# Kernel optimization log

Hardware: AMD Instinct MI355X
Metric: run time of the kernel (lower is better)

The kernel has to match this reference:

```python
import jax, jax.numpy as jnp
import numpy as np

D_MODEL = 1024
H = 16
D_K = D_MODEL // H  # 64


def setup_inputs() -> dict:
    key = jax.random.key(0)
    ks = jax.random.split(key, 10)
    s = 1.0 / np.sqrt(D_MODEL)
    x = jax.random.normal(ks[0], (4, 2048, D_MODEL), dtype=jnp.float32)
    # Per-head linear weights stacked: [H, d_model, d_k]
    Wq = jax.random.uniform(ks[1], (H, D_MODEL, D_K), jnp.float32, -s, s)
    bq = jax.random.uniform(ks[2], (H, D_K), jnp.float32, -s, s)
    Wk = jax.random.uniform(ks[3], (H, D_MODEL, D_K), jnp.float32, -s, s)
    bk = jax.random.uniform(ks[4], (H, D_K), jnp.float32, -s, s)
    Wv = jax.random.uniform(ks[5], (H, D_MODEL, D_K), jnp.float32, -s, s)
    bv = jax.random.uniform(ks[6], (H, D_K), jnp.float32, -s, s)
    so = 1.0 / np.sqrt(H * D_K)
    Wo = jax.random.uniform(ks[7], (H * D_K, D_MODEL), jnp.float32, -so, so)
    bo = jax.random.uniform(ks[8], (D_MODEL,), jnp.float32, -so, so)
    return {"x": x, "Wq": Wq, "bq": bq, "Wk": Wk, "bk": bk, "Wv": Wv, "bv": bv, "Wo": Wo, "bo": bo}


def reference(x, Wq, bq, Wk, bk, Wv, bv, Wo, bo):
    # x: [B, S, D]; Wq/Wk/Wv: [H, D, d_k]; b*: [H, d_k]
    q = jnp.einsum('bsd,hdk->bhsk', x, Wq) + bq[None, :, None, :]
    k = jnp.einsum('bsd,hdk->bhsk', x, Wk) + bk[None, :, None, :]
    v = jnp.einsum('bsd,hdk->bhsk', x, Wv) + bv[None, :, None, :]
    scores = jnp.einsum('bhqk,bhsk->bhqs', q, k) / np.sqrt(D_K)
    S = x.shape[1]
    causal = jnp.triu(jnp.ones((S, S), dtype=bool), k=1)  # True above diagonal
    scores = jnp.where(causal, -jnp.inf, scores)
    attn = jax.nn.softmax(scores, axis=-1)
    ctx = jnp.einsum('bhqs,bhsk->bhqk', attn, v)  # [B, H, S, d_k]
    B = x.shape[0]
    # concat heads: torch cats head outputs along last dim -> [B, S, H*d_k]
    ctx = jnp.transpose(ctx, (0, 2, 1, 3)).reshape(B, S, H * D_K)
    return ctx @ Wo + bo
```

## Files before the change

kernel.cpp:

```cpp
#include <hip/hip_runtime.h>
#include <hip/hip_bf16.h>

typedef unsigned short u16;
typedef __attribute__((ext_vector_type(8))) short short8;
typedef __attribute__((ext_vector_type(4))) short short4v;
typedef __attribute__((ext_vector_type(4))) float floatx4;

#define D_MODEL 1024
#define NH 16
#define SEQ 2048
#define BATCH 4
#define M_ROWS 8192
#define N_QKV 3072

#define QSCALE 0.18033688011112042f
#define EXP2_OFF 11.541560327111707f

__device__ __forceinline__ u16 f2u(float f) {
    __hip_bfloat16 h = __float2bfloat16(f);
    u16 u; __builtin_memcpy(&u, &h, 2); return u;
}

__device__ __forceinline__ void async_copy16(const u16* g, u16* l) {
    __builtin_amdgcn_global_load_lds(
        (const __attribute__((address_space(1))) unsigned int*)(g),
        (__attribute__((address_space(3))) unsigned int*)(l),
        16, 0, 0);
}

__global__ __launch_bounds__(256) void prep(
    const float* __restrict__ x,
    const float* __restrict__ Wq, const float* __restrict__ Wk,
    const float* __restrict__ Wv, const float* __restrict__ Wo,
    const float* __restrict__ bq, const float* __restrict__ bk,
    const float* __restrict__ bv, const float* __restrict__ bo,
    u16* __restrict__ xb, u16* __restrict__ Wpt, u16* __restrict__ Wot,
    float* __restrict__ biasp)
{
    __shared__ u16 T[64 * 72];
    const int tid = threadIdx.x;
    const int blk = blockIdx.x;

    if (blk < 4096) {
        size_t i = ((size_t)blk * 256 + tid) * 8;
        float4 f0 = *(const float4*)&x[i];
        float4 f1 = *(const float4*)&x[i + 4];
        u16 t[8] = {f2u(f0.x), f2u(f0.y), f2u(f0.z), f2u(f0.w),
                    f2u(f1.x), f2u(f1.y), f2u(f1.z), f2u(f1.w)};
        *(short8*)&xb[i] = *(short8*)t;
        return;
    }
    if (blk == 5120) {
        #pragma unroll
        for (int j = 0; j < 16; j++) {
            int idx = j * 256 + tid;
            float v;
            if (idx < 1024)      v = bq[idx] * QSCALE;
            else if (idx < 2048) v = bk[idx - 1024];
            else if (idx < 3072) v = bv[idx - 2048];
            else                 v = bo[idx - 3072];
            biasp[idx] = v;
        }
        return;
    }
    const int wb = blk - 4096;
    const int r = tid >> 2, s4 = (tid & 3) * 16;
    if (wb < 768) {
        int sel = wb / 256, rem = wb % 256;
        int h = rem >> 4, ktile = rem & 15;
        const float* W = (sel == 0) ? Wq : ((sel == 1) ? Wk : Wv);
        const float scale = (sel == 0) ? QSCALE : 1.0f;
        const float* src = W + ((size_t)h * 1024 + ktile * 64 + r) * 64 + s4;
        #pragma unroll
        for (int i = 0; i < 16; i++) T[(s4 + i) * 72 + r] = f2u(src[i] * scale);
        __syncthreads();
        u16 tmp[16];
        #pragma unroll
        for (int i = 0; i < 16; i++) tmp[i] = T[r * 72 + s4 + i];
        u16* dst = Wpt + ((size_t)sel * 1024 + h * 64 + r) * 1024 + ktile * 64 + s4;
        *(short8*)&dst[0] = *(short8*)&tmp[0];
        *(short8*)&dst[8] = *(short8*)&tmp[8];
    } else {
        int rem = wb - 768;
        int nt = rem >> 4, kt2 = rem & 15;
        const float* src = Wo + ((size_t)kt2 * 64 + r) * 1024 + nt * 64 + s4;
        #pragma unroll
        for (int i = 0; i < 16; i++) T[(s4 + i) * 72 + r] = f2u(src[i]);
        __syncthreads();
        u16 tmp[16];
        #pragma unroll
        for (int i = 0; i < 16; i++) tmp[i] = T[r * 72 + s4 + i];
        u16* dst = Wot + ((size_t)nt * 64 + r) * 1024 + kt2 * 64 + s4;
        *(short8*)&dst[0] = *(short8*)&tmp[0];
        *(short8*)&dst[8] = *(short8*)&tmp[8];
    }
}

__global__ __launch_bounds__(256) void vtrans(const u16* __restrict__ QKV,
                                              u16* __restrict__ Vtg) {
    __shared__ u16 T[64 * 72];
    const int bh = blockIdx.x, kt = blockIdx.y;
    const int b = bh >> 4, h = bh & 15;
    const int tid = threadIdx.x;
    const int r = tid >> 2, s4 = (tid & 3) * 16;
    const u16* vp = QKV + (size_t)(b * SEQ + kt * 64 + r) * N_QKV + 2 * D_MODEL + h * 64 + s4;
    *(short8*)&T[r * 72 + s4]     = *(const short8*)&vp[0];
    *(short8*)&T[r * 72 + s4 + 8] = *(const short8*)&vp[8];
    __syncthreads();
    u16 tmp[16];
    #pragma unroll
    for (int i = 0; i < 16; i++) tmp[i] = T[(s4 + i) * 72 + r];
    u16* op = Vtg + ((size_t)bh * 64 + r) * SEQ + kt * 64 + s4;
    *(short8*)&op[0] = *(short8*)&tmp[0];
    *(short8*)&op[8] = *(short8*)&tmp[8];
}

#define G256_BAR   __builtin_amdgcn_s_barrier()
#define G256_LGKM(n) { asm volatile("s_waitcnt lgkmcnt(" #n ")" ::: "memory"); \
                       __builtin_amdgcn_sched_barrier(0); }

#define GQ_STAGE_A(bb, ca, kq) \
    async_copy16(pAc + (size_t)(ca) * 64 * K + (kq), \
                 &lds[(bb) * 28672 + (ca) * 4096 + stw]);

#define GQ_STAGE_B(bb, cb, kq) \
    async_copy16(pBc + (size_t)(cb) * 64 * K + (kq), \
                 &lds[(bb) * 28672 + 16384 + (cb) * 4096 + stw]);

#define GQ_LDA4(dst, bb, mi0) { \
    const int _b = (bb) * 28672 + wm * 8192; \
    _Pragma("unroll") \
    for (int mi = 0; mi < 4; mi++) { \
        const int _r = _b + (((mi0) + mi) * 16 + l16) * 64; \
        dst[mi * 2]     = *(const short8*)&lds[_r + col0]; \
        dst[mi * 2 + 1] = *(const short8*)&lds[_r + col1]; \
    } }

#define GQ_LDB2(dst, bb, ni0) { \
    const int _b = (bb) * 28672 + 16384 + wn * 3072; \
    _Pragma("unroll") \
    for (int ni = 0; ni < 2; ni++) { \
        const int _r = _b + (((ni0) + ni) * 16 + l16) * 64; \
        dst[ni * 2]     = *(const short8*)&lds[_r + col0]; \
        dst[ni * 2 + 1] = *(const short8*)&lds[_r + col1]; \
    } }

#define GQ_LDB1(dst, bb, ni0) { \
    const int _b = (bb) * 28672 + 16384 + wn * 3072; \
    const int _r = _b + ((ni0) * 16 + l16) * 64; \
    dst[0] = *(const short8*)&lds[_r + col0]; \
    dst[1] = *(const short8*)&lds[_r + col1]; }

#define GQ_MMA8(av, bv, MI0, NI0) { \
    _Pragma("unroll") \
    for (int mi = 0; mi < 4; mi++) \
    _Pragma("unroll") \
    for (int ni = 0; ni < 2; ni++) { \
        acc[(MI0) + mi][(NI0) + ni] = __builtin_amdgcn_mfma_f32_16x16x32_bf16( \
            bv[ni * 2],     av[mi * 2],     acc[(MI0) + mi][(NI0) + ni], 0, 0, 0); \
        acc[(MI0) + mi][(NI0) + ni] = __builtin_amdgcn_mfma_f32_16x16x32_bf16( \
            bv[ni * 2 + 1], av[mi * 2 + 1], acc[(MI0) + mi][(NI0) + ni], 0, 0, 0); \
    } }

#define GQ_MMA4(av, bv, MI0) { \
    _Pragma("unroll") \
    for (int mi = 0; mi < 4; mi++) { \
        acc[(MI0) + mi][2] = __builtin_amdgcn_mfma_f32_16x16x32_bf16( \
            bv[0], av[mi * 2],     acc[(MI0) + mi][2], 0, 0, 0); \
        acc[(MI0) + mi][2] = __builtin_amdgcn_mfma_f32_16x16x32_bf16( \
            bv[1], av[mi * 2 + 1], acc[(MI0) + mi][2], 0, 0, 0); \
    } }

template <typename OT>
__global__ __launch_bounds__(512, 2) void gemm_qkv(
    const u16* __restrict__ A, const u16* __restrict__ Bt,
    const float* __restrict__ bias, OT* __restrict__ C,
    int M, int N, int K)
{
    __shared__ u16 lds[57344];
    const int tid = threadIdx.x;
    const int w = tid >> 6, lane = tid & 63;
    const int l16 = lane & 15, quad = lane >> 4;
    const int wm = w >> 2, wn = w & 3;

    const int nwgx = gridDim.x;
    const int nwg = nwgx * gridDim.y;
    const int lin = blockIdx.y * nwgx + blockIdx.x;
    const int cpx = nwg >> 3;
    const int swz = (lin & 7) * cpx + (lin >> 3);
    const int bn = (swz % nwgx) * 192, bm = (swz / nwgx) * 256;

    const int d = tid * 16;
    const int s = d ^ (((d >> 7) & 7) << 4);
    const int r = s >> 7;
    const int c = (s & 127) >> 1;
    const u16* pAc = A  + (size_t)(bm + r) * K + c;
    const u16* pBc = Bt + (size_t)(bn + r) * K + c;
    const int stw = w * 512;

    const int xm = (l16 & 7) << 3;
    const int col0 = (quad * 8) ^ xm;
    const int col1 = (32 + quad * 8) ^ xm;

    floatx4 acc[8][3];
    #pragma unroll
    for (int i = 0; i < 8; i++)
        #pragma unroll
        for (int j = 0; j < 3; j++) acc[i][j] = (floatx4){0.f, 0.f, 0.f, 0.f};

    GQ_STAGE_A(0, 0, 0); GQ_STAGE_A(0, 1, 0); GQ_STAGE_A(0, 2, 0); GQ_STAGE_A(0, 3, 0);
    GQ_STAGE_B(0, 0, 0); GQ_STAGE_B(0, 1, 0); GQ_STAGE_B(0, 2, 0);
    GQ_STAGE_B(1, 0, 64); GQ_STAGE_B(1, 1, 64); GQ_STAGE_B(1, 2, 64);
    asm volatile("s_waitcnt vmcnt(3)" ::: "memory");
    __syncthreads();

    short8 a0[8], a1[8], b0[4], b1[2];
    GQ_LDA4(a0, 0, 0);
    GQ_LDB2(b0, 0, 0);

    const int NKT = K >> 6;
    for (int kt = 0; kt < NKT; ++kt) {
        const int buf = kt & 1, nb = buf ^ 1;
        const int kqA = (kt + 1) << 6, kqB = (kt + 2) << 6;
        const bool st1 = (kt + 1 < NKT), st2 = (kt + 2 < NKT);

        GQ_LDB1(b1, buf, 2);
        if (st1) { GQ_STAGE_A(nb, 0, kqA); GQ_STAGE_A(nb, 1, kqA); }
        G256_BAR; G256_LGKM(2);
        __builtin_amdgcn_s_setprio(1); GQ_MMA8(a0, b0, 0, 0);
        __builtin_amdgcn_s_setprio(0); G256_BAR;

        GQ_LDA4(a1, buf, 4);
        if (st1) { GQ_STAGE_A(nb, 2, kqA); GQ_STAGE_A(nb, 3, kqA); }
        G256_BAR; G256_LGKM(8);
        __builtin_amdgcn_s_setprio(1); GQ_MMA4(a0, b1, 0);
        __builtin_amdgcn_s_setprio(0); G256_BAR;

        if (st2) { GQ_STAGE_B(buf, 0, kqB); GQ_STAGE_B(buf, 1, kqB); }
        G256_BAR; G256_LGKM(0);
        __builtin_amdgcn_s_setprio(1); GQ_MMA8(a1, b0, 4, 0);
        __builtin_amdgcn_s_setprio(0); G256_BAR;

        if (st2) { GQ_STAGE_B(buf, 2, kqB); }
        if (st1) {
            if (st2) { asm volatile("s_waitcnt vmcnt(3)" ::: "memory"); }
            else     { asm volatile("s_waitcnt vmcnt(0)" ::: "memory"); }
            __builtin_amdgcn_sched_barrier(0);
            GQ_LDA4(a0, nb, 0);
            GQ_LDB2(b0, nb, 0);
        }
        G256_BAR;
        __builtin_amdgcn_s_setprio(1); GQ_MMA4(a1, b1, 4);
        __builtin_amdgcn_s_setprio(0); G256_BAR;
    }

    float4 bi[3];
    #pragma unroll
    for (int ni = 0; ni < 3; ni++)
        bi[ni] = *(const float4*)&bias[bn + wn * 48 + ni * 16 + quad * 4];
    #pragma unroll
    for (int mi = 0; mi < 8; mi++) {
        const int row = bm + wm * 128 + mi * 16 + l16;
        #pragma unroll
        for (int ni = 0; ni < 3; ni++) {
            const int col = bn + wn * 48 + ni * 16 + quad * 4;
            const float v0 = acc[mi][ni][0] + bi[ni].x;
            const float v1 = acc[mi][ni][1] + bi[ni].y;
            const float v2 = acc[mi][ni][2] + bi[ni].z;
            const float v3 = acc[mi][ni][3] + bi[ni].w;
            if constexpr (sizeof(OT) == 2) {
                u16 o[4] = {f2u(v0), f2u(v1), f2u(v2), f2u(v3)};
                *(short4v*)&((u16*)C)[(size_t)row * N + col] = *(short4v*)o;
            } else {
                float4 fv = {v0, v1, v2, v3};
                *(float4*)&C[(size_t)row * N + col] = fv;
            }
        }
    }
}

#define GO_STAGE_A(bb, ca, kq) \
    async_copy16(pAc + (size_t)(ca) * 64 * K + (kq), \
                 &lds[(bb) * 24576 + (ca) * 4096 + stw]);

#define GO_STAGE_B(bb, cb, kq) \
    async_copy16(pBc + (size_t)(cb) * 64 * K + (kq), \
                 &lds[(bb) * 24576 + 16384 + (cb) * 4096 + stw]);

#define GO_LDA4(dst, bb, mi0) { \
    const int _b = (bb) * 24576 + wm * 8192; \
    _Pragma("unroll") \
    for (int mi = 0; mi < 4; mi++) { \
        const int _r = _b + (((mi0) + mi) * 16 + l16) * 64; \
        dst[mi * 2]     = *(const short8*)&lds[_r + col0]; \
        dst[mi * 2 + 1] = *(const short8*)&lds[_r + col1]; \
    } }

#define GO_LDB1(dst, bb, ni) { \
    const int _b = (bb) * 24576 + 16384; \
    const int _r = _b + (wn * 32 + (ni) * 16 + l16) * 64; \
    dst[0] = *(const short8*)&lds[_r + col0]; \
    dst[1] = *(const short8*)&lds[_r + col1]; }

#define GO_MMA(av, bv, MI0, NI) { \
    _Pragma("unroll") \
    for (int mi = 0; mi < 4; mi++) { \
        acc[(MI0) + mi][NI] = __builtin_amdgcn_mfma_f32_16x16x32_bf16( \
            bv[0], av[mi * 2],     acc[(MI0) + mi][NI], 0, 0, 0); \
        acc[(MI0) + mi][NI] = __builtin_amdgcn_mfma_f32_16x16x32_bf16( \
            bv[1], av[mi * 2 + 1], acc[(MI0) + mi][NI], 0, 0, 0); \
    } }

__global__ __launch_bounds__(512, 2) void gemm_out(
    const u16* __restrict__ A, const u16* __restrict__ Bt,
    const float* __restrict__ bias, float* __restrict__ C,
    int M, int N, int K)
{
    __shared__ u16 lds[49152];
    const int tid = threadIdx.x;
    const int w = tid >> 6, lane = tid & 63;
    const int l16 = lane & 15, quad = lane >> 4;
    const int wm = w >> 2, wn = w & 3;

    const int nwgx = gridDim.x;
    const int nwg = nwgx * gridDim.y;
    const int lin = blockIdx.y * nwgx + blockIdx.x;
    const int cpx = nwg >> 3;
    const int swz = (lin & 7) * cpx + (lin >> 3);
    const int bn = (swz % nwgx) * 128, bm = (swz / nwgx) * 256;

    const int d = tid * 16;
    const int s = d ^ (((d >> 7) & 7) << 4);
    const int r = s >> 7;
    const int c = (s & 127) >> 1;
    const u16* pAc = A  + (size_t)(bm + r) * K + c;
    const u16* pBc = Bt + (size_t)(bn + r) * K + c;
    const int stw = w * 512;

    const int xm = (l16 & 7) << 3;
    const int col0 = (quad * 8) ^ xm;
    const int col1 = (32 + quad * 8) ^ xm;

    floatx4 acc[8][2];
    #pragma unroll
    for (int i = 0; i < 8; i++)
        #pragma unroll
        for (int j = 0; j < 2; j++) acc[i][j] = (floatx4){0.f, 0.f, 0.f, 0.f};

    GO_STAGE_A(0, 0, 0); GO_STAGE_A(0, 1, 0); GO_STAGE_A(0, 2, 0); GO_STAGE_A(0, 3, 0);
    GO_STAGE_B(0, 0, 0); GO_STAGE_B(0, 1, 0);
    GO_STAGE_B(1, 0, 64); GO_STAGE_B(1, 1, 64);
    asm volatile("s_waitcnt vmcnt(2)" ::: "memory");
    __syncthreads();

    short8 a0[8], a1[8], bb0[2], bb1[2];
    GO_LDA4(a0, 0, 0);
    GO_LDB1(bb0, 0, 0);

    const int NKT = K >> 6;
    for (int kt = 0; kt < NKT; ++kt) {
        const int buf = kt & 1, nb = buf ^ 1;
        const int kqA = (kt + 1) << 6, kqB = (kt + 2) << 6;
        const bool st1 = (kt + 1 < NKT), st2 = (kt + 2 < NKT);

        GO_LDB1(bb1, buf, 1);
        if (st1) { GO_STAGE_A(nb, 0, kqA); GO_STAGE_A(nb, 1, kqA); }
        G256_BAR; G256_LGKM(2);
        __builtin_amdgcn_s_setprio(1); GO_MMA(a0, bb0, 0, 0);
        __builtin_amdgcn_s_setprio(0); G256_BAR;

        GO_LDA4(a1, buf, 4);
        if (st1) { GO_STAGE_A(nb, 2, kqA); GO_STAGE_A(nb, 3, kqA); }
        G256_BAR; G256_LGKM(8);
        __builtin_amdgcn_s_setprio(1); GO_MMA(a0, bb1, 0, 1);
        __builtin_amdgcn_s_setprio(0); G256_BAR;

        if (st2) { GO_STAGE_B(buf, 0, kqB); GO_STAGE_B(buf, 1, kqB); }
        G256_BAR; G256_LGKM(0);
        __builtin_amdgcn_s_setprio(1); GO_MMA(a1, bb0, 4, 0);
        __builtin_amdgcn_s_setprio(0); G256_BAR;

        if (st1) {
            if (st2) { asm volatile("s_waitcnt vmcnt(2)" ::: "memory"); }
            else     { asm volatile("s_waitcnt vmcnt(0)" ::: "memory"); }
            __builtin_amdgcn_sched_barrier(0);
            GO_LDA4(a0, nb, 0);
            GO_LDB1(bb0, nb, 0);
        }
        G256_BAR;
        __builtin_amdgcn_s_setprio(1); GO_MMA(a1, bb1, 4, 1);
        __builtin_amdgcn_s_setprio(0); G256_BAR;
    }

    float4 bi[2];
    #pragma unroll
    for (int ni = 0; ni < 2; ni++)
        bi[ni] = *(const float4*)&bias[bn + wn * 32 + ni * 16 + quad * 4];
    #pragma unroll
    for (int mi = 0; mi < 8; mi++) {
        const int row = bm + wm * 128 + mi * 16 + l16;
        #pragma unroll
        for (int ni = 0; ni < 2; ni++) {
            const int col = bn + wn * 32 + ni * 16 + quad * 4;
            float4 fv = {acc[mi][ni][0] + bi[ni].x, acc[mi][ni][1] + bi[ni].y,
                         acc[mi][ni][2] + bi[ni].z, acc[mi][ni][3] + bi[ni].w};
            *(float4*)&C[(size_t)row * N + col] = fv;
        }
    }
}

__global__ __launch_bounds__(256) void attn_mfma(
    const u16* __restrict__ QKV, const u16* __restrict__ Vtg, u16* __restrict__ ctx)
{
    __shared__ u16 Ks[2][64 * 64];
    __shared__ u16 Vs[2][64 * 64];
    __shared__ u16 Ps[4 * 16 * 64];

    const int bh = blockIdx.x;
    const int qt = (int)(gridDim.y - 1) - (int)blockIdx.y;
    const int b = bh >> 4, h = bh & 15;
    const int tid = threadIdx.x;
    const int w = tid >> 6, lane = tid & 63;
    const int l16 = lane & 15, quad = lane >> 4;

    const int r0 = tid >> 3,        c0 = tid & 7;
    const int r1 = (256 + tid) >> 3, c1 = tid & 7;
    const int sw0 = c0 ^ (r0 & 7), sw1 = c1 ^ (r1 & 7);

    short8 q[2][2];
    #pragma unroll
    for (int m = 0; m < 2; m++) {
        const u16* qp = QKV + (size_t)(b * SEQ + qt * 128 + w * 32 + m * 16 + l16) * N_QKV + h * 64;
        q[m][0] = *(const short8*)&qp[quad * 8];
        q[m][1] = *(const short8*)&qp[32 + quad * 8];
    }

    short8 ones8;
    #pragma unroll
    for (int i = 0; i < 8; i++) ones8[i] = (short)0x3F80;

    floatx4 O[2][4];
    floatx4 lsum[2];
    #pragma unroll
    for (int m = 0; m < 2; m++) {
        lsum[m] = (floatx4){0.f, 0.f, 0.f, 0.f};
        #pragma unroll
        for (int i = 0; i < 4; i++) O[m][i] = (floatx4){0.f, 0.f, 0.f, 0.f};
    }

    const int nkt = 2 * qt + 2;
    const int qrow_w_max = qt * 128 + w * 32 + 31;

    const size_t kbase = (size_t)(b * SEQ) * N_QKV + D_MODEL + h * 64;
    const size_t vbase = (size_t)bh * 64 * SEQ;

    const u16* kpa = QKV + kbase + (size_t)r0 * N_QKV + c0 * 8;
    const u16* kpb = QKV + kbase + (size_t)r1 * N_QKV + c1 * 8;
    const u16* vpa = Vtg + vbase + (size_t)r0 * SEQ + c0 * 8;
    const u16* vpb = Vtg + vbase + (size_t)r1 * SEQ + c1 * 8;

    {
        float4 ka = *(const float4*)kpa;
        float4 kb = *(const float4*)kpb;
        float4 va = *(const float4*)vpa;
        float4 vb = *(const float4*)vpb;
        *(float4*)&Ks[0][r0 * 64 + sw0 * 8] = ka;
        *(float4*)&Ks[0][r1 * 64 + sw1 * 8] = kb;
        *(float4*)&Vs[0][r0 * 64 + sw0 * 8] = va;
        *(float4*)&Vs[0][r1 * 64 + sw1 * 8] = vb;
    }
    kpa += (size_t)64 * N_QKV; kpb += (size_t)64 * N_QKV;
    vpa += 64; vpb += 64;
    __syncthreads();

    const int e7 = l16 & 7;
    const int pbase = w * 1024 + l16 * 64;

    for (int kt = 0; kt < nkt; kt++) {
        const int buf = kt & 1;
        const bool pre = (kt + 1 < nkt);
        float4 ka, kb, va, vb;
        if (pre) {
            ka = *(const float4*)kpa;
            kb = *(const float4*)kpb;
            va = *(const float4*)vpa;
            vb = *(const float4*)vpb;
            kpa += (size_t)64 * N_QKV; kpb += (size_t)64 * N_QKV;
            vpa += 64; vpb += 64;
        }

        if (kt * 64 <= qrow_w_max) {
            short8 kf[4][2];
            #pragma unroll
            for (int ns = 0; ns < 4; ns++) {
                const int rr = ns * 16 + l16, rs = rr & 7;
                kf[ns][0] = *(short8*)&Ks[buf][rr * 64 + (quad ^ rs) * 8];
                kf[ns][1] = *(short8*)&Ks[buf][rr * 64 + ((4 + quad) ^ rs) * 8];
            }
            const bool needMask = (kt * 64 + 63 > qt * 128 + w * 32);

            floatx4 z[2][4];
            __builtin_amdgcn_s_setprio(1);
            #pragma unroll
            for (int m = 0; m < 2; m++)
                #pragma unroll
                for (int ns = 0; ns < 4; ns++) {
                    floatx4 t = (floatx4){0.f, 0.f, 0.f, 0.f};
                    t = __builtin_amdgcn_mfma_f32_16x16x32_bf16(kf[ns][0], q[m][0], t, 0, 0, 0);
                    t = __builtin_amdgcn_mfma_f32_16x16x32_bf16(kf[ns][1], q[m][1], t, 0, 0, 0);
                    z[m][ns] = t;
                }
            __builtin_amdgcn_s_setprio(0);

            short8 vf[4][2];
            #pragma unroll
            for (int ds = 0; ds < 4; ds++) {
                const int rr = ds * 16 + l16, rs = rr & 7;
                vf[ds][0] = *(short8*)&Vs[buf][rr * 64 + (quad ^ rs) * 8];
                vf[ds][1] = *(short8*)&Vs[buf][rr * 64 + ((4 + quad) ^ rs) * 8];
            }

            #pragma unroll
            for (int m = 0; m < 2; m++) {
                const int qrow_g = qt * 128 + w * 32 + m * 16 + l16;
                #pragma unroll
                for (int ns = 0; ns < 4; ns++) {
                    u16 pk[4];
                    #pragma unroll
                    for (int r = 0; r < 4; r++) {
                        float s = z[m][ns][r];
                        const int key = kt * 64 + ns * 16 + quad * 4 + r;
                        if (needMask && key > qrow_g) s = -INFINITY;
                        float p = __builtin_amdgcn_exp2f(s - EXP2_OFF);
                        pk[r] = f2u(p);
                    }
                    *(short4v*)&Ps[pbase + (((ns * 4 + quad) ^ (2 * e7)) << 2)] = *(short4v*)pk;
                }
                short8 p0 = *(short8*)&Ps[pbase + ((quad ^ e7) << 3)];
                short8 p1 = *(short8*)&Ps[pbase + (((4 + quad) ^ e7) << 3)];
                __builtin_amdgcn_s_setprio(1);
                lsum[m] = __builtin_amdgcn_mfma_f32_16x16x32_bf16(ones8, p0, lsum[m], 0, 0, 0);
                lsum[m] = __builtin_amdgcn_mfma_f32_16x16x32_bf16(ones8, p1, lsum[m], 0, 0, 0);
                #pragma unroll
                for (int ds = 0; ds < 4; ds++) {
                    O[m][ds] = __builtin_amdgcn_mfma_f32_16x16x32_bf16(vf[ds][0], p0, O[m][ds], 0, 0, 0);
                    O[m][ds] = __builtin_amdgcn_mfma_f32_16x16x32_bf16(vf[ds][1], p1, O[m][ds], 0, 0, 0);
                }
                __builtin_amdgcn_s_setprio(0);
            }
        }

        if (pre) {
            const int nb = buf ^ 1;
            *(float4*)&Ks[nb][r0 * 64 + sw0 * 8] = ka;
            *(float4*)&Ks[nb][r1 * 64 + sw1 * 8] = kb;
            *(float4*)&Vs[nb][r0 * 64 + sw0 * 8] = va;
            *(float4*)&Vs[nb][r1 * 64 + sw1 * 8] = vb;
        }
        __syncthreads();
    }

    #pragma unroll
    for (int m = 0; m < 2; m++) {
        const float inv = 1.0f / lsum[m][0];
        const size_t base = (size_t)(b * SEQ + qt * 128 + w * 32 + m * 16 + l16) * D_MODEL + h * 64;
        #pragma unroll
        for (int ds = 0; ds < 4; ds++) {
            u16 o[4];
            #pragma unroll
            for (int r = 0; r < 4; r++) o[r] = f2u(O[m][ds][r] * inv);
            *(short4v*)&ctx[base + ds * 16 + quad * 4] = *(short4v*)o;
        }
    }
}

extern "C" void kernel_launch(void* const* d_in, const int* in_sizes, int n_in,
                              void* d_out, int out_size, void* d_ws, size_t ws_size,
                              hipStream_t stream) {
    const float* x  = (const float*)d_in[0];
    const float* Wq = (const float*)d_in[1];
    const float* bq = (const float*)d_in[2];
    const float* Wk = (const float*)d_in[3];
    const float* bk = (const float*)d_in[4];
    const float* Wv = (const float*)d_in[5];
    const float* bv = (const float*)d_in[6];
    const float* Wo = (const float*)d_in[7];
    const float* bo = (const float*)d_in[8];
    float* out = (float*)d_out;

    char* ws = (char*)d_ws;
    float* biasp = (float*)ws;
    u16*   Wpt   = (u16*)(ws + 0x10000);
    u16*   Wot   = (u16*)(ws + 0x620000);
    u16*   xb    = (u16*)(ws + 0x840000);
    u16*   Vtg   = xb;
    u16*   QKV   = (u16*)(ws + 0x1840000);
    u16*   ctx   = (u16*)(ws + 0x4840000);

    prep<<<5121, 256, 0, stream>>>(x, Wq, Wk, Wv, Wo, bq, bk, bv, bo,
                                   xb, Wpt, Wot, biasp);

    gemm_qkv<u16><<<dim3(N_QKV / 192, M_ROWS / 256), 512, 0, stream>>>(
        xb, Wpt, biasp, QKV, M_ROWS, N_QKV, D_MODEL);

    vtrans<<<dim3(64, 32), 256, 0, stream>>>(QKV, Vtg);

    attn_mfma<<<dim3(BATCH * NH, SEQ / 128), 256, 0, stream>>>(QKV, Vtg, ctx);

    gemm_out<<<dim3(D_MODEL / 128, M_ROWS / 256), 512, 0, stream>>>(
        ctx, Wot, biasp + N_QKV, out, M_ROWS, D_MODEL, D_MODEL);
}
```

Measured before the change: 277.7 us.

## Fuse V transpose into QKV GEMM epilogue and restructure attention P staging

The QKV GEMM epilogue now writes the V columns straight into a per-head transposed layout, which removes the separate vtrans kernel and its extra global read and write. Q and K are stored in a narrower 2048-column buffer. In attention, P is computed per m and written to a padded, unswizzled LDS tile (stride 72), and the PV MFMAs then run in one high-priority block. The transposed V stores are scalar 2-byte writes spread across rows SEQ apart, which are poorly coalesced and may slow the GEMM epilogue.

```diff
diff --git a/kernel.cpp b/kernel.cpp
--- a/kernel.cpp
+++ b/kernel.cpp
@@ -12,6 +12,8 @@
 #define BATCH 4
 #define M_ROWS 8192
 #define N_QKV 3072
+#define N_QK 2048
+#define PS_LD 72
 
 #define QSCALE 0.18033688011112042f
 #define EXP2_OFF 11.541560327111707f
@@ -96,25 +98,6 @@
     }
 }
 
-__global__ __launch_bounds__(256) void vtrans(const u16* __restrict__ QKV,
-                                              u16* __restrict__ Vtg) {
-    __shared__ u16 T[64 * 72];
-    const int bh = blockIdx.x, kt = blockIdx.y;
-    const int b = bh >> 4, h = bh & 15;
-    const int tid = threadIdx.x;
-    const int r = tid >> 2, s4 = (tid & 3) * 16;
-    const u16* vp = QKV + (size_t)(b * SEQ + kt * 64 + r) * N_QKV + 2 * D_MODEL + h * 64 + s4;
-    *(short8*)&T[r * 72 + s4]     = *(const short8*)&vp[0];
-    *(short8*)&T[r * 72 + s4 + 8] = *(const short8*)&vp[8];
-    __syncthreads();
-    u16 tmp[16];
-    #pragma unroll
-    for (int i = 0; i < 16; i++) tmp[i] = T[(s4 + i) * 72 + r];
-    u16* op = Vtg + ((size_t)bh * 64 + r) * SEQ + kt * 64 + s4;
-    *(short8*)&op[0] = *(short8*)&tmp[0];
-    *(short8*)&op[8] = *(short8*)&tmp[8];
-}
-
 #define G256_BAR   __builtin_amdgcn_s_barrier()
 #define G256_LGKM(n) { asm volatile("s_waitcnt lgkmcnt(" #n ")" ::: "memory"); \
                        __builtin_amdgcn_sched_barrier(0); }
@@ -171,11 +154,10 @@
             bv[1], av[mi * 2 + 1], acc[(MI0) + mi][2], 0, 0, 0); \
     } }
 
-template <typename OT>
 __global__ __launch_bounds__(512, 2) void gemm_qkv(
     const u16* __restrict__ A, const u16* __restrict__ Bt,
-    const float* __restrict__ bias, OT* __restrict__ C,
-    int M, int N, int K)
+    const float* __restrict__ bias, u16* __restrict__ C,
+    u16* __restrict__ Vtg, int M, int N, int K)
 {
     __shared__ u16 lds[57344];
     const int tid = threadIdx.x;
@@ -263,17 +245,24 @@
         const int row = bm + wm * 128 + mi * 16 + l16;
         #pragma unroll
         for (int ni = 0; ni < 3; ni++) {
-            const int col = bn + wn * 48 + ni * 16 + quad * 4;
+            const int colbase = bn + wn * 48 + ni * 16;
+            const int col = colbase + quad * 4;
             const float v0 = acc[mi][ni][0] + bi[ni].x;
             const float v1 = acc[mi][ni][1] + bi[ni].y;
             const float v2 = acc[mi][ni][2] + bi[ni].z;
             const float v3 = acc[mi][ni][3] + bi[ni].w;
-            if constexpr (sizeof(OT) == 2) {
+            if (colbase < 2048) {
                 u16 o[4] = {f2u(v0), f2u(v1), f2u(v2), f2u(v3)};
-                *(short4v*)&((u16*)C)[(size_t)row * N + col] = *(short4v*)o;
+                *(short4v*)&C[(size_t)row * N_QK + col] = *(short4v*)o;
             } else {
-                float4 fv = {v0, v1, v2, v3};
-                *(float4*)&C[(size_t)row * N + col] = fv;
+                const int dh = col - 2048;
+                const size_t vrow =
+                    ((size_t)((row >> 11) * 16 + (dh >> 6)) * 64 + (dh & 63)) * SEQ
+                    + (row & 2047);
+                Vtg[vrow]            = f2u(v0);
+                Vtg[vrow + SEQ]      = f2u(v1);
+                Vtg[vrow + 2 * SEQ]  = f2u(v2);
+                Vtg[vrow + 3 * SEQ]  = f2u(v3);
             }
         }
     }
@@ -410,11 +399,11 @@
 }
 
 __global__ __launch_bounds__(256) void attn_mfma(
-    const u16* __restrict__ QKV, const u16* __restrict__ Vtg, u16* __restrict__ ctx)
+    const u16* __restrict__ QK, const u16* __restrict__ Vtg, u16* __restrict__ ctx)
 {
     __shared__ u16 Ks[2][64 * 64];
     __shared__ u16 Vs[2][64 * 64];
-    __shared__ u16 Ps[4 * 16 * 64];
+    __shared__ u16 Ps[128 * PS_LD];
 
     const int bh = blockIdx.x;
     const int qt = (int)(gridDim.y - 1) - (int)blockIdx.y;
@@ -430,7 +419,7 @@
     short8 q[2][2];
     #pragma unroll
     for (int m = 0; m < 2; m++) {
-        const u16* qp = QKV + (size_t)(b * SEQ + qt * 128 + w * 32 + m * 16 + l16) * N_QKV + h * 64;
+        const u16* qp = QK + (size_t)(b * SEQ + qt * 128 + w * 32 + m * 16 + l16) * N_QK + h * 64;
         q[m][0] = *(const short8*)&qp[quad * 8];
         q[m][1] = *(const short8*)&qp[32 + quad * 8];
     }
@@ -451,11 +440,11 @@
     const int nkt = 2 * qt + 2;
     const int qrow_w_max = qt * 128 + w * 32 + 31;
 
-    const size_t kbase = (size_t)(b * SEQ) * N_QKV + D_MODEL + h * 64;
+    const size_t kbase = (size_t)(b * SEQ) * N_QK + D_MODEL + h * 64;
     const size_t vbase = (size_t)bh * 64 * SEQ;
 
-    const u16* kpa = QKV + kbase + (size_t)r0 * N_QKV + c0 * 8;
-    const u16* kpb = QKV + kbase + (size_t)r1 * N_QKV + c1 * 8;
+    const u16* kpa = QK + kbase + (size_t)r0 * N_QK + c0 * 8;
+    const u16* kpb = QK + kbase + (size_t)r1 * N_QK + c1 * 8;
     const u16* vpa = Vtg + vbase + (size_t)r0 * SEQ + c0 * 8;
     const u16* vpb = Vtg + vbase + (size_t)r1 * SEQ + c1 * 8;
 
@@ -469,12 +458,9 @@
         *(float4*)&Vs[0][r0 * 64 + sw0 * 8] = va;
         *(float4*)&Vs[0][r1 * 64 + sw1 * 8] = vb;
     }
-    kpa += (size_t)64 * N_QKV; kpb += (size_t)64 * N_QKV;
+    kpa += (size_t)64 * N_QK; kpb += (size_t)64 * N_QK;
     vpa += 64; vpb += 64;
     __syncthreads();
-
-    const int e7 = l16 & 7;
-    const int pbase = w * 1024 + l16 * 64;
 
     for (int kt = 0; kt < nkt; kt++) {
         const int buf = kt & 1;
@@ -485,7 +471,7 @@
             kb = *(const float4*)kpb;
             va = *(const float4*)vpa;
             vb = *(const float4*)vpb;
-            kpa += (size_t)64 * N_QKV; kpb += (size_t)64 * N_QKV;
+            kpa += (size_t)64 * N_QK; kpb += (size_t)64 * N_QK;
             vpa += 64; vpb += 64;
         }
 
@@ -499,18 +485,34 @@
             }
             const bool needMask = (kt * 64 + 63 > qt * 128 + w * 32);
 
-            floatx4 z[2][4];
-            __builtin_amdgcn_s_setprio(1);
             #pragma unroll
-            for (int m = 0; m < 2; m++)
+            for (int m = 0; m < 2; m++) {
+                floatx4 z[4];
+                __builtin_amdgcn_s_setprio(1);
                 #pragma unroll
                 for (int ns = 0; ns < 4; ns++) {
                     floatx4 t = (floatx4){0.f, 0.f, 0.f, 0.f};
                     t = __builtin_amdgcn_mfma_f32_16x16x32_bf16(kf[ns][0], q[m][0], t, 0, 0, 0);
                     t = __builtin_amdgcn_mfma_f32_16x16x32_bf16(kf[ns][1], q[m][1], t, 0, 0, 0);
-                    z[m][ns] = t;
+                    z[ns] = t;
                 }
-            __builtin_amdgcn_s_setprio(0);
+                __builtin_amdgcn_s_setprio(0);
+                const int qrow_g = qt * 128 + w * 32 + m * 16 + l16;
+                const int prow = (w * 32 + m * 16 + l16) * PS_LD;
+                #pragma unroll
+                for (int ns = 0; ns < 4; ns++) {
+                    u16 pk[4];
+                    #pragma unroll
+                    for (int r = 0; r < 4; r++) {
+                        float s = z[ns][r];
+                        const int key = kt * 64 + ns * 16 + quad * 4 + r;
+                        if (needMask && key > qrow_g) s = -INFINITY;
+                        float p = __builtin_amdgcn_exp2f(s - EXP2_OFF);
+                        pk[r] = f2u(p);
+                    }
+                    *(short4v*)&Ps[prow + ns * 16 + quad * 4] = *(short4v*)pk;
+                }
+            }
 
             short8 vf[4][2];
             #pragma unroll
@@ -519,26 +521,12 @@
                 vf[ds][0] = *(short8*)&Vs[buf][rr * 64 + (quad ^ rs) * 8];
                 vf[ds][1] = *(short8*)&Vs[buf][rr * 64 + ((4 + quad) ^ rs) * 8];
             }
-
+            __builtin_amdgcn_s_setprio(1);
             #pragma unroll
             for (int m = 0; m < 2; m++) {
-                const int qrow_g = qt * 128 + w * 32 + m * 16 + l16;
-                #pragma unroll
-                for (int ns = 0; ns < 4; ns++) {
-                    u16 pk[4];
-                    #pragma unroll
-                    for (int r = 0; r < 4; r++) {
-                        float s = z[m][ns][r];
-                        const int key = kt * 64 + ns * 16 + quad * 4 + r;
-                        if (needMask && key > qrow_g) s = -INFINITY;
-                        float p = __builtin_amdgcn_exp2f(s - EXP2_OFF);
-                        pk[r] = f2u(p);
-                    }
-                    *(short4v*)&Ps[pbase + (((ns * 4 + quad) ^ (2 * e7)) << 2)] = *(short4v*)pk;
-                }
-                short8 p0 = *(short8*)&Ps[pbase + ((quad ^ e7) << 3)];
-                short8 p1 = *(short8*)&Ps[pbase + (((4 + quad) ^ e7) << 3)];
-                __builtin_amdgcn_s_setprio(1);
+                const int prow = (w * 32 + m * 16 + l16) * PS_LD;
+                short8 p0 = *(short8*)&Ps[prow + quad * 8];
+                short8 p1 = *(short8*)&Ps[prow + 32 + quad * 8];
                 lsum[m] = __builtin_amdgcn_mfma_f32_16x16x32_bf16(ones8, p0, lsum[m], 0, 0, 0);
                 lsum[m] = __builtin_amdgcn_mfma_f32_16x16x32_bf16(ones8, p1, lsum[m], 0, 0, 0);
                 #pragma unroll
@@ -546,8 +534,8 @@
                     O[m][ds] = __builtin_amdgcn_mfma_f32_16x16x32_bf16(vf[ds][0], p0, O[m][ds], 0, 0, 0);
                     O[m][ds] = __builtin_amdgcn_mfma_f32_16x16x32_bf16(vf[ds][1], p1, O[m][ds], 0, 0, 0);
                 }
-                __builtin_amdgcn_s_setprio(0);
             }
+            __builtin_amdgcn_s_setprio(0);
         }
 
         if (pre) {
@@ -593,19 +581,17 @@
     u16*   Wpt   = (u16*)(ws + 0x10000);
     u16*   Wot   = (u16*)(ws + 0x620000);
     u16*   xb    = (u16*)(ws + 0x840000);
-    u16*   Vtg   = xb;
-    u16*   QKV   = (u16*)(ws + 0x1840000);
+    u16*   QK    = (u16*)(ws + 0x1840000);
+    u16*   Vtg   = (u16*)(ws + 0x3840000);
     u16*   ctx   = (u16*)(ws + 0x4840000);
 
     prep<<<5121, 256, 0, stream>>>(x, Wq, Wk, Wv, Wo, bq, bk, bv, bo,
                                    xb, Wpt, Wot, biasp);
 
-    gemm_qkv<u16><<<dim3(N_QKV / 192, M_ROWS / 256), 512, 0, stream>>>(
-        xb, Wpt, biasp, QKV, M_ROWS, N_QKV, D_MODEL);
-
-    vtrans<<<dim3(64, 32), 256, 0, stream>>>(QKV, Vtg);
-
-    attn_mfma<<<dim3(BATCH * NH, SEQ / 128), 256, 0, stream>>>(QKV, Vtg, ctx);
+    gemm_qkv<<<dim3(N_QKV / 192, M_ROWS / 256), 512, 0, stream>>>(
+        xb, Wpt, biasp, QK, Vtg, M_ROWS, N_QKV, D_MODEL);
+
+    attn_mfma<<<dim3(BATCH * NH, SEQ / 128), 256, 0, stream>>>(QK, Vtg, ctx);
 
     gemm_out<<<dim3(D_MODEL / 128, M_ROWS / 256), 512, 0, stream>>>(
         ctx, Wot, biasp + N_QKV, out, M_ROWS, D_MODEL, D_MODEL);
```

Result: faster. 256.7 us (-7.6%).
